# Kernel optimization log

Measured on AMD Instinct MI355X. Metric: run time of the kernel, lower is better.

Reference implementation:

```python
import jax, jax.numpy as jnp
import numpy as np

B, Q, C, H, N, D, F = 1, 2048, 2048, 1024, 16, 64, 4096
R = Q + C  # relative position encoding length
EPS = 1e-12
NEG = 1e30


def setup_inputs() -> dict:
    key = jax.random.key(0)
    ks = jax.random.split(key, 16)
    s = 0.02
    return dict(
        content_stream=jax.random.normal(ks[0], (B, Q, H), jnp.float32),
        content_mask=jnp.zeros((B, 1, Q, C), jnp.float32),
        context=jax.random.normal(ks[1], (B, C, H), jnp.float32),
        position_encoding=jax.random.normal(ks[2], (B, R, H), jnp.float32),
        content_bias=jax.random.normal(ks[3], (N, D), jnp.float32) * s,
        position_bias=jax.random.normal(ks[4], (N, D), jnp.float32) * s,
        segment_encoding=jax.random.normal(ks[5], (2, N, D), jnp.float32) * s,
        segment_matrix=jax.random.randint(ks[6], (B, Q, C), 0, 2).astype(bool),
        segment_bias=jax.random.normal(ks[7], (N, D), jnp.float32) * s,
        Wq=jax.random.normal(ks[8], (H, N, D), jnp.float32) * s,
        Wk=jax.random.normal(ks[9], (H, N, D), jnp.float32) * s,
        Wv=jax.random.normal(ks[10], (H, N, D), jnp.float32) * s,
        Wr=jax.random.normal(ks[11], (H, N, D), jnp.float32) * s,
        Wo=jax.random.normal(ks[12], (H, N, D), jnp.float32) * s,
        ln1_gamma=jnp.ones((H,), jnp.float32),
        ln1_beta=jnp.zeros((H,), jnp.float32),
        W1=jax.random.normal(ks[13], (H, F), jnp.float32) * s,
        b1=jnp.zeros((F,), jnp.float32),
        W2=jax.random.normal(ks[14], (F, H), jnp.float32) * s,
        b2=jnp.zeros((H,), jnp.float32),
        ln2_gamma=jnp.ones((H,), jnp.float32),
        ln2_beta=jnp.zeros((H,), jnp.float32),
    )


def _layernorm(x, g, b):
    m = jnp.mean(x, axis=-1, keepdims=True)
    v = jnp.mean(jnp.square(x - m), axis=-1, keepdims=True)
    return (x - m) * jax.lax.rsqrt(v + EPS) * g + b


def _rel_shift(x, klen):
    # x: [b, n, q, r] -> shifted [b, n, q, klen] (XLNet reshape trick)
    b, n, q, r = x.shape
    x = x.reshape(b, n, r, q)[:, :, 1:, :].reshape(b, n, q, r - 1)
    return x[:, :, :, :klen]


def reference(content_stream, content_mask, context, position_encoding,
              content_bias, position_bias, segment_encoding, segment_matrix,
              segment_bias, Wq, Wk, Wv, Wr, Wo, ln1_gamma, ln1_beta,
              W1, b1, W2, b2, ln2_gamma, ln2_beta):
    q = jnp.einsum('bqh,hnd->bqnd', content_stream, Wq)
    k = jnp.einsum('bch,hnd->bcnd', context, Wk)
    v = jnp.einsum('bch,hnd->bcnd', context, Wv)
    r = jnp.einsum('brh,hnd->brnd', position_encoding, Wr)

    # content / position / segment bias terms (XLNet relative attention)
    ac = jnp.einsum('bqnd,bcnd->bnqc', q + content_bias, k)
    bd = _rel_shift(jnp.einsum('bqnd,brnd->bnqr', q + position_bias, r),
                    k.shape[1])
    ef = jnp.einsum('bqnd,snd->bnqs', q + segment_bias, segment_encoding)
    ef = jnp.where(segment_matrix[:, None], ef[..., 1:], ef[..., :1])

    scores = (ac + bd + ef) / jnp.sqrt(jnp.float32(D))
    scores = scores - NEG * content_mask  # mask: 1.0 = disallowed
    probs = jax.nn.softmax(scores, axis=-1)

    attn = jnp.einsum('bnqc,bcnd->bqnd', probs, v)
    attn_out = jnp.einsum('bqnd,hnd->bqh', attn, Wo)

    # residual + LN, then FFN, residual + LN (dropout off: training=False)
    ffn_in = _layernorm(attn_out + content_stream, ln1_gamma, ln1_beta)
    ffn_out = jax.nn.relu(ffn_in @ W1 + b1) @ W2 + b2
    return _layernorm(ffn_out + ffn_in, ln2_gamma, ln2_beta)
```

## Files before the change

### kernel.cpp

```cpp
#include <hip/hip_runtime.h>
#include <stdint.h>


typedef unsigned short ushort_t;
typedef __attribute__((ext_vector_type(8))) short bf16x8;
typedef __attribute__((ext_vector_type(4))) float f32x4;

#define QLEN 2048
#define CLEN 2048
#define HDIM 1024
#define NHEAD 16
#define DHEAD 64
#define RLEN 4096
#define FDIM 4096

__device__ __forceinline__ float bf2f(ushort_t u) {
  union { float f; uint32_t i; } x; x.i = ((uint32_t)u) << 16; return x.f;
}
__device__ __forceinline__ ushort_t f2bf(float f) {
  union { float f; uint32_t i; } x; x.f = f;
  uint32_t r = x.i + 0x7fffu + ((x.i >> 16) & 1u);
  return (ushort_t)(r >> 16);
}
__device__ __forceinline__ f32x4 mfma16(bf16x8 a, bf16x8 b, f32x4 c) {
  return __builtin_amdgcn_mfma_f32_16x16x32_bf16(a, b, c, 0, 0, 0);
}
__device__ __forceinline__ bool probe_bf16(const uint32_t* probe) {
  return probe[0] == 0x3F803F80u;
}

typedef const __attribute__((address_space(1))) void* gas_t;
typedef __attribute__((address_space(3))) void* las_t;
__device__ __forceinline__ void glds16(const void* g, void* l) {
  __builtin_amdgcn_global_load_lds((gas_t)(uintptr_t)g, (las_t)(uintptr_t)l, 16, 0, 0);
}

__device__ __forceinline__ void bar_lds() {
  __asm__ volatile("s_waitcnt lgkmcnt(0)\n\ts_barrier" ::: "memory");
}
__device__ __forceinline__ void bar_full() {
  __asm__ volatile("s_waitcnt vmcnt(0) lgkmcnt(0)\n\ts_barrier" ::: "memory");
}

struct ConvJobs {
  const void* src[5];
  const void* mask_src;
  ushort_t* dst[5];
  int n[5];
  int blk0[6];
};

__global__ __launch_bounds__(256) void conv_all(
    ConvJobs J, const uint32_t* __restrict__ probe)
{
  const bool isb = probe_bf16(probe);
  int j = 0;
  #pragma unroll
  for (int t = 1; t < 5; t++) if ((int)blockIdx.x >= J.blk0[t]) j = t;
  const int lb = blockIdx.x - J.blk0[j];
  const int nb = J.blk0[j + 1] - J.blk0[j];
  const int n = J.n[j];
  ushort_t* dst = J.dst[j];
  if (j < 4) {
    const void* src = J.src[j];
    for (int i = lb * 256 + threadIdx.x; i < n; i += nb * 256)
      dst[i] = isb ? ((const ushort_t*)src)[i] : f2bf(((const float*)src)[i]);
  } else {
    const void* sm = J.src[4];
    uint32_t sw = 0;
    #pragma unroll
    for (int t = 0; t < 8; t++) sw |= ((const uint32_t*)sm)[t];
    const bool i8 = sw > 1u;
    for (int i = lb * 256 + threadIdx.x; i < n; i += nb * 256) {
      const int s = i8 ? (int)((const unsigned char*)sm)[i]
                       : (int)((const uint32_t*)sm)[i];
      const float mv = isb ? bf2f(((const ushort_t*)J.mask_src)[i])
                           : ((const float*)J.mask_src)[i];
      const float f = (float)(s ? 1 : 0) + (mv != 0.f ? 2.f : 0.f);
      dst[i] = f2bf(f);
    }
  }
}

struct SmallBatch {
  const void* src[10];
  int n[10];
  int off[10];
};

__global__ __launch_bounds__(256) void convert_small(
    SmallBatch sb, ushort_t* __restrict__ dst, const uint32_t* __restrict__ probe)
{
  const bool isb = probe_bf16(probe);
  const int t = blockIdx.x;
  const void* s = sb.src[t];
  ushort_t* d = dst + sb.off[t];
  for (int i = threadIdx.x; i < sb.n[t]; i += 256)
    d[i] = isb ? ((const ushort_t*)s)[i] : f2bf(((const float*)s)[i]);
}

struct TransJobs { const void* src[4]; ushort_t* dst[4]; };
__global__ __launch_bounds__(256) void transpose4_to_bf16(
    TransJobs T, int R, int C, const uint32_t* __restrict__ probe)
{
  const bool isb = probe_bf16(probe);
  const void* in = T.src[blockIdx.z];
  ushort_t* out = T.dst[blockIdx.z];
  __shared__ ushort_t t[32][33];
  const int bx = blockIdx.x * 32, by = blockIdx.y * 32;
  const int x = threadIdx.x & 31, y0 = threadIdx.x >> 5;
  #pragma unroll
  for (int yy = 0; yy < 32; yy += 8) {
    const size_t idx = (size_t)(by + y0 + yy) * C + bx + x;
    t[y0 + yy][x] = isb ? ((const ushort_t*)in)[idx] : f2bf(((const float*)in)[idx]);
  }
  __syncthreads();
  #pragma unroll
  for (int yy = 0; yy < 32; yy += 8)
    out[(size_t)(bx + y0 + yy) * R + by + x] = t[x][y0 + yy];
}

__global__ __launch_bounds__(256) void transpose_to_bf16(
    const void* __restrict__ in, ushort_t* __restrict__ out, int R, int C,
    const uint32_t* __restrict__ probe)
{
  const bool isb = probe_bf16(probe);
  __shared__ ushort_t t[32][33];
  const int bx = blockIdx.x * 32, by = blockIdx.y * 32;
  const int x = threadIdx.x & 31, y0 = threadIdx.x >> 5;
  #pragma unroll
  for (int yy = 0; yy < 32; yy += 8) {
    const size_t idx = (size_t)(by + y0 + yy) * C + bx + x;
    t[y0 + yy][x] = isb ? ((const ushort_t*)in)[idx] : f2bf(((const float*)in)[idx]);
  }
  __syncthreads();
  #pragma unroll
  for (int yy = 0; yy < 32; yy += 8)
    out[(size_t)(bx + y0 + yy) * R + by + x] = t[x][y0 + yy];
}

__device__ __forceinline__ void gemm_store(
    void* out, const ushort_t* bias, int M, int N, int epi,
    int gm, int gn, float v)
{
  if (epi == 0) {
    ((ushort_t*)out)[(size_t)gm * N + gn] = f2bf(v);
  } else if (epi == 1) {
    ((ushort_t*)out)[(size_t)gn * M + gm] = f2bf(v);
  } else if (epi == 2) {
    ((float*)out)[(size_t)gm * N + gn] = v;
  } else if (epi == 3) {
    v += bf2f(bias[gn]); v = v > 0.f ? v : 0.f;
    ((ushort_t*)out)[(size_t)gm * N + gn] = f2bf(v);
  } else if (epi == 4) {
    v += bf2f(bias[gn]);
    ((float*)out)[(size_t)gm * N + gn] = v;
  } else {
    ((ushort_t*)out)[((size_t)(gn >> 6) * M + gm) * 64 + (gn & 63)] = f2bf(v);
  }
}

__global__ __launch_bounds__(256) void gemm_bt_kernel(
    const ushort_t* __restrict__ A, const ushort_t* __restrict__ Bt,
    const ushort_t* __restrict__ bias, void* __restrict__ out,
    int M, int N, int K, int epi)
{
  __shared__ __attribute__((aligned(16))) ushort_t As[128 * 32];
  __shared__ __attribute__((aligned(16))) ushort_t Bs[64 * 32];
  const int tid = threadIdx.x;
  const int lane = tid & 63, wave = tid >> 6;
  const int l15 = lane & 15, quad = lane >> 4;
  const int m0 = blockIdx.y * 128, n0 = blockIdx.x * 64;

  const int arow = tid >> 2;
  const int acol = (tid & 3) * 8;

  f32x4 acc[2][4];
  #pragma unroll
  for (int i = 0; i < 2; i++)
    #pragma unroll
    for (int j = 0; j < 4; j++) acc[i][j] = (f32x4){0.f, 0.f, 0.f, 0.f};

  for (int k0 = 0; k0 < K; k0 += 32) {
    glds16(&A[(size_t)(m0 + arow) * K + k0 + acol], &As[tid * 8]);
    glds16(&A[(size_t)(m0 + arow + 64) * K + k0 + acol], &As[tid * 8 + 2048]);
    glds16(&Bt[(size_t)(n0 + arow) * K + k0 + acol], &Bs[tid * 8]);
    __syncthreads();
    bf16x8 af[2], bfr[4];
    #pragma unroll
    for (int i = 0; i < 2; i++)
      af[i] = *(const bf16x8*)&As[(wave * 32 + i * 16 + l15) * 32 + quad * 8];
    #pragma unroll
    for (int j = 0; j < 4; j++)
      bfr[j] = *(const bf16x8*)&Bs[(j * 16 + l15) * 32 + quad * 8];
    #pragma unroll
    for (int i = 0; i < 2; i++)
      #pragma unroll
      for (int j = 0; j < 4; j++)
        acc[i][j] = mfma16(af[i], bfr[j], acc[i][j]);
    __syncthreads();
  }

  #pragma unroll
  for (int i = 0; i < 2; i++)
    #pragma unroll
    for (int j = 0; j < 4; j++)
      #pragma unroll
      for (int rg = 0; rg < 4; rg++)
        gemm_store(out, bias, M, N, epi,
                   m0 + wave * 32 + i * 16 + quad * 4 + rg,
                   n0 + j * 16 + l15, acc[i][j][rg]);
}

__global__ __launch_bounds__(256) void gemm64_bt_kernel(
    const ushort_t* __restrict__ A, const ushort_t* __restrict__ Bt,
    const ushort_t* __restrict__ bias, void* __restrict__ out,
    int M, int N, int K, int epi)
{
  __shared__ __attribute__((aligned(16))) ushort_t As[64 * 32];
  __shared__ __attribute__((aligned(16))) ushort_t Bs[64 * 32];
  const int tid = threadIdx.x;
  const int lane = tid & 63, wave = tid >> 6;
  const int l15 = lane & 15, quad = lane >> 4;
  const int wm = wave >> 1, wn = wave & 1;
  const int m0 = blockIdx.y * 64, n0 = blockIdx.x * 64;

  const int arow = tid >> 2;
  const int acol = (tid & 3) * 8;

  f32x4 acc[2][2];
  #pragma unroll
  for (int i = 0; i < 2; i++)
    #pragma unroll
    for (int j = 0; j < 2; j++) acc[i][j] = (f32x4){0.f, 0.f, 0.f, 0.f};

  for (int k0 = 0; k0 < K; k0 += 32) {
    glds16(&A[(size_t)(m0 + arow) * K + k0 + acol], &As[tid * 8]);
    glds16(&Bt[(size_t)(n0 + arow) * K + k0 + acol], &Bs[tid * 8]);
    __syncthreads();
    bf16x8 af[2], bfr[2];
    #pragma unroll
    for (int i = 0; i < 2; i++)
      af[i] = *(const bf16x8*)&As[(wm * 32 + i * 16 + l15) * 32 + quad * 8];
    #pragma unroll
    for (int j = 0; j < 2; j++)
      bfr[j] = *(const bf16x8*)&Bs[(wn * 32 + j * 16 + l15) * 32 + quad * 8];
    #pragma unroll
    for (int i = 0; i < 2; i++)
      #pragma unroll
      for (int j = 0; j < 2; j++)
        acc[i][j] = mfma16(af[i], bfr[j], acc[i][j]);
    __syncthreads();
  }

  #pragma unroll
  for (int i = 0; i < 2; i++)
    #pragma unroll
    for (int j = 0; j < 2; j++)
      #pragma unroll
      for (int rg = 0; rg < 4; rg++)
        gemm_store(out, bias, M, N, epi,
                   m0 + wm * 32 + i * 16 + quad * 4 + rg,
                   n0 + wn * 32 + j * 16 + l15, acc[i][j][rg]);
}

#define ESTR 36
#define PSTR2 72
__global__ __launch_bounds__(256, 2) void attn_flash(
    const ushort_t* __restrict__ qh, const ushort_t* __restrict__ kh,
    const ushort_t* __restrict__ vT, const ushort_t* __restrict__ rh,
    const ushort_t* __restrict__ cbias, const ushort_t* __restrict__ pbias,
    const ushort_t* __restrict__ sbias, const ushort_t* __restrict__ senc,
    const ushort_t* __restrict__ fmb, ushort_t* __restrict__ attn)
{
  __shared__ __attribute__((aligned(16))) ushort_t kbuf[2][64 * 64];
  __shared__ __attribute__((aligned(16))) ushort_t vbuf[2][64 * 64];
  __shared__ __attribute__((aligned(16))) ushort_t rbuf[2][80 * 64];
  __shared__ __attribute__((aligned(16))) ushort_t Pbuf[16 * PSTR2];
  __shared__ __attribute__((aligned(16))) float escr[4][16 * ESTR];
  __shared__ __attribute__((aligned(16))) ushort_t qpc[16 * 64];
  __shared__ __attribute__((aligned(16))) ushort_t qpp[16 * 64];
  __shared__ float wsum[4][16];
  __shared__ float e0s[16], e1s[16];

  const int n = blockIdx.x;
  const int q0 = blockIdx.y * 16;
  const int tid = threadIdx.x;
  const int lane = tid & 63, wave = tid >> 6;
  const int l15 = lane & 15, quad = lane >> 4;

  const ushort_t* qn = qh + (size_t)n * QLEN * 64;
  const ushort_t* kn = kh + (size_t)n * CLEN * 64;
  const ushort_t* rn = rh + (size_t)n * RLEN * 64;
  const ushort_t* vn = vT + (size_t)n * 64 * CLEN;

  const int srow = lane >> 3;
  const int sg = (lane & 7) ^ srow;

  for (int idx = tid; idx < 16 * 64; idx += 256) {
    const int row = idx >> 6, col = idx & 63;
    const float qv = bf2f(qn[(size_t)(q0 + row) * 64 + col]);
    qpc[idx] = f2bf(qv + bf2f(cbias[n * DHEAD + col]));
    qpp[idx] = f2bf(qv + bf2f(pbias[n * DHEAD + col]));
  }
  if (tid < 32) {
    const int row = tid & 15, sidx = tid >> 4;
    float a = 0.f;
    for (int d = 0; d < DHEAD; d++)
      a += (bf2f(qn[(size_t)(q0 + row) * 64 + d]) + bf2f(sbias[n * DHEAD + d]))
           * bf2f(senc[(size_t)(sidx * NHEAD + n) * DHEAD + d]);
    if (sidx == 0) e0s[row] = a; else e1s[row] = a;
  }

  {
    const int c0 = 0, ua = c0 - q0 + (QLEN - 16);
    if (wave == 0) {
      #pragma unroll
      for (int i = 0; i < 8; i++)
        glds16(kn + (size_t)(c0 + i * 8 + srow) * 64 + sg * 8, &kbuf[0][i * 512]);
    } else if (wave == 1) {
      #pragma unroll
      for (int i = 0; i < 8; i++)
        glds16(vn + (size_t)(i * 8 + srow) * CLEN + c0 + sg * 8, &vbuf[0][i * 512]);
    } else if (wave == 2) {
      #pragma unroll
      for (int i = 0; i < 8; i++)
        glds16(rn + (size_t)(ua + i * 8 + srow) * 64 + sg * 8, &rbuf[0][i * 512]);
    } else {
      #pragma unroll
      for (int i = 0; i < 2; i++)
        glds16(rn + (size_t)(ua + 64 + i * 8 + srow) * 64 + sg * 8, &rbuf[0][(64 + i * 8) * 64]);
    }
  }
  bar_full();

  const bf16x8* qpc8 = (const bf16x8*)qpc;
  const bf16x8* qpp8 = (const bf16x8*)qpp;
  const bf16x8 qc0 = qpc8[l15 * 8 + quad];
  const bf16x8 qc1 = qpc8[l15 * 8 + 4 + quad];
  const bf16x8 qp0 = qpp8[l15 * 8 + quad];
  const bf16x8 qp1 = qpp8[l15 * 8 + 4 + quad];
  const float a0_ = e0s[l15] * 0.125f;
  const float ad_ = (e1s[l15] - e0s[l15]) * 0.125f;

  float* escr_w = escr[wave];
  const int gk0 = quad ^ (l15 & 7);
  const int gk1 = (quad + 4) ^ (l15 & 7);

  float l_row = 0.f;
  f32x4 O = (f32x4){0.f, 0.f, 0.f, 0.f};

  for (int ci = 0; ci < CLEN / 64; ci++) {
    const int b = ci & 1;
    const int c0 = ci * 64;

    if (ci + 1 < CLEN / 64) {
      const int c1 = c0 + 64, ua1 = c1 - q0 + (QLEN - 16);
      if (wave == 0) {
        #pragma unroll
        for (int i = 0; i < 8; i++)
          glds16(kn + (size_t)(c1 + i * 8 + srow) * 64 + sg * 8, &kbuf[b ^ 1][i * 512]);
      } else if (wave == 1) {
        #pragma unroll
        for (int i = 0; i < 8; i++)
          glds16(vn + (size_t)(i * 8 + srow) * CLEN + c1 + sg * 8, &vbuf[b ^ 1][i * 512]);
      } else if (wave == 2) {
        #pragma unroll
        for (int i = 0; i < 8; i++)
          glds16(rn + (size_t)(ua1 + i * 8 + srow) * 64 + sg * 8, &rbuf[b ^ 1][i * 512]);
      } else {
        #pragma unroll
        for (int i = 0; i < 2; i++)
          glds16(rn + (size_t)(ua1 + 64 + i * 8 + srow) * 64 + sg * 8, &rbuf[b ^ 1][(64 + i * 8) * 64]);
      }
    }

    const size_t eoff = (size_t)(q0 + l15) * CLEN + c0 + wave * 16 + quad * 4;
    const uint2 fmv = *(const uint2*)&fmb[eoff];

    #pragma unroll
    for (int t = 0; t < 2; t++) {
      const int rrow = (wave + t) * 16 + l15;
      f32x4 e = (f32x4){0.f, 0.f, 0.f, 0.f};
      e = mfma16(*(const bf16x8*)&rbuf[b][rrow * 64 + gk0 * 8], qp0, e);
      e = mfma16(*(const bf16x8*)&rbuf[b][rrow * 64 + gk1 * 8], qp1, e);
      *(f32x4*)&escr_w[l15 * ESTR + t * 16 + quad * 4] = e;
    }

    const int krow = wave * 16 + l15;
    f32x4 a = (f32x4){0.f, 0.f, 0.f, 0.f};
    a = mfma16(*(const bf16x8*)&kbuf[b][krow * 64 + gk0 * 8], qc0, a);
    a = mfma16(*(const bf16x8*)&kbuf[b][krow * 64 + gk1 * 8], qc1, a);

    const ushort_t fm4[4] = {(ushort_t)(fmv.x & 0xffff), (ushort_t)(fmv.x >> 16),
                             (ushort_t)(fmv.y & 0xffff), (ushort_t)(fmv.y >> 16)};
    const float* dg = &escr_w[l15 * ESTR + quad * 4 - l15 + 16];
    float p[4], psum = 0.f;
    #pragma unroll
    for (int rg = 0; rg < 4; rg++) {
      const float f = bf2f(fm4[rg]);
      const float mk = floorf(f * 0.5f);
      const float sm = f - 2.f * mk;
      float v = fmaf(a[rg] + dg[rg], 0.125f, fmaf(sm, ad_, a0_));
      v = fmaf(mk, -1.0e30f, v);
      p[rg] = __expf(v);
      psum += p[rg];
    }
    psum += __shfl_xor(psum, 16);
    psum += __shfl_xor(psum, 32);
    l_row += psum;

    {
      uint2 pk;
      pk.x = (uint32_t)f2bf(p[0]) | ((uint32_t)f2bf(p[1]) << 16);
      pk.y = (uint32_t)f2bf(p[2]) | ((uint32_t)f2bf(p[3]) << 16);
      *(uint2*)&Pbuf[l15 * PSTR2 + wave * 16 + quad * 4] = pk;
    }
    bar_lds();

    const bf16x8 pa0 = *(const bf16x8*)&Pbuf[l15 * PSTR2 + quad * 8];
    const bf16x8 pa1 = *(const bf16x8*)&Pbuf[l15 * PSTR2 + 32 + quad * 8];
    const int vrow = wave * 16 + l15;
    O = mfma16(pa0, *(const bf16x8*)&vbuf[b][vrow * 64 + gk0 * 8], O);
    O = mfma16(pa1, *(const bf16x8*)&vbuf[b][vrow * 64 + gk1 * 8], O);

    bar_full();
  }

  if (quad == 0) wsum[wave][l15] = l_row;
  __syncthreads();
  const float l = wsum[0][l15] + wsum[1][l15] + wsum[2][l15] + wsum[3][l15];
  const float linv = 1.0f / l;
  float linv4[4];
  #pragma unroll
  for (int rg = 0; rg < 4; rg++) linv4[rg] = __shfl(linv, quad * 4 + rg);
  #pragma unroll
  for (int rg = 0; rg < 4; rg++)
    attn[(size_t)(q0 + quad * 4 + rg) * HDIM + n * 64 + wave * 16 + l15] =
        f2bf(O[rg] * linv4[rg]);
}

__global__ __launch_bounds__(256) void ln_kernel(
    const float* __restrict__ x, const ushort_t* __restrict__ res_bf,
    const float* __restrict__ res_f, const ushort_t* __restrict__ gamma,
    const ushort_t* __restrict__ beta, ushort_t* __restrict__ out_bf,
    float* __restrict__ out_f, void* __restrict__ out_dyn,
    const uint32_t* __restrict__ probe)
{
  const int row = blockIdx.x, tid = threadIdx.x;
  const int lane = tid & 63, wave = tid >> 6;
  __shared__ float red[8];
  const size_t base = (size_t)row * HDIM;
  float v[4];
  #pragma unroll
  for (int i = 0; i < 4; i++) {
    const int h = tid + i * 256;
    const float rv = res_bf ? bf2f(res_bf[base + h]) : res_f[base + h];
    v[i] = x[base + h] + rv;
  }
  float s = v[0] + v[1] + v[2] + v[3];
  float ss = v[0] * v[0] + v[1] * v[1] + v[2] * v[2] + v[3] * v[3];
  #pragma unroll
  for (int off = 32; off > 0; off >>= 1) {
    s += __shfl_xor(s, off);
    ss += __shfl_xor(ss, off);
  }
  if (lane == 0) { red[wave] = s; red[4 + wave] = ss; }
  __syncthreads();
  s = red[0] + red[1] + red[2] + red[3];
  ss = red[4] + red[5] + red[6] + red[7];
  const float mean = s * (1.0f / HDIM);
  float var = ss * (1.0f / HDIM) - mean * mean;
  var = var > 0.f ? var : 0.f;
  const float rs = rsqrtf(var + 1e-12f);
  const bool outb = out_dyn ? probe_bf16(probe) : false;
  #pragma unroll
  for (int i = 0; i < 4; i++) {
    const int h = tid + i * 256;
    const float y = (v[i] - mean) * rs * bf2f(gamma[h]) + bf2f(beta[h]);
    if (out_bf) out_bf[base + h] = f2bf(y);
    if (out_f)  out_f[base + h] = y;
    if (out_dyn) {
      if (outb) ((ushort_t*)out_dyn)[base + h] = f2bf(y);
      else      ((float*)out_dyn)[base + h] = y;
    }
  }
}

extern "C" void kernel_launch(void* const* d_in, const int* in_sizes, int n_in,
                              void* d_out, int out_size, void* d_ws, size_t ws_size,
                              hipStream_t stream)
{
  (void)in_sizes; (void)n_in; (void)out_size; (void)ws_size;

  const void* cs_r   = d_in[0];
  const void* mask_r = d_in[1];
  const void* ctx_r  = d_in[2];
  const void* pe_r   = d_in[3];
  const void* cb_r   = d_in[4];
  const void* pb_r   = d_in[5];
  const void* senc_r = d_in[6];
  const void* smat   = d_in[7];
  const void* sb_r   = d_in[8];
  const void* Wq_r   = d_in[9];
  const void* Wk_r   = d_in[10];
  const void* Wv_r   = d_in[11];
  const void* Wr_r   = d_in[12];
  const void* Wo_r   = d_in[13];
  const void* g1_r   = d_in[14];
  const void* be1_r  = d_in[15];
  const void* W1_r   = d_in[16];
  const void* b1_r   = d_in[17];
  const void* W2_r   = d_in[18];
  const void* b2_r   = d_in[19];
  const void* g2_r   = d_in[20];
  const void* be2_r  = d_in[21];

  const uint32_t* probe = (const uint32_t*)g1_r;

  char* w = (char*)d_ws;
  #define WSOFF(mb) ((void*)(w + ((size_t)(mb) << 20)))
  ushort_t* fm_b     = (ushort_t*)WSOFF(0);
  ushort_t* Wqt      = (ushort_t*)WSOFF(8);
  ushort_t* Wkt      = (ushort_t*)WSOFF(10);
  ushort_t* Wvt      = (ushort_t*)WSOFF(12);
  ushort_t* Wrt      = (ushort_t*)WSOFF(14);
  ushort_t* W1t      = (ushort_t*)WSOFF(16);
  ushort_t* W2t      = (ushort_t*)WSOFF(24);
  ushort_t* Wo_b     = (ushort_t*)WSOFF(32);
  ushort_t* smalls   = (ushort_t*)WSOFF(34);
  ushort_t* cs_b     = (ushort_t*)WSOFF(35);
  ushort_t* ctx_b    = (ushort_t*)WSOFF(47);
  ushort_t* pe_b     = (ushort_t*)WSOFF(51);
  ushort_t* qbuf     = (ushort_t*)WSOFF(59);
  ushort_t* kbuf     = (ushort_t*)WSOFF(63);
  ushort_t* vTbuf    = (ushort_t*)WSOFF(67);
  ushort_t* rbuf     = (ushort_t*)WSOFF(71);
  ushort_t* attnbuf  = (ushort_t*)WSOFF(79);
  float*    attn_out = (float*)WSOFF(83);
  ushort_t* ffn_in_b = (ushort_t*)WSOFF(91);
  ushort_t* hidden   = (ushort_t*)WSOFF(39);
  float*    ffn_in_f = (float*)WSOFF(71);
  float*    ffn_out  = (float*)WSOFF(83);

  ushort_t* cb   = smalls + 0;
  ushort_t* pb   = smalls + 1024;
  ushort_t* sb   = smalls + 2048;
  ushort_t* senc = smalls + 3072;
  ushort_t* b1   = smalls + 5120;
  ushort_t* b2   = smalls + 9216;
  ushort_t* g1   = smalls + 10240;
  ushort_t* be1  = smalls + 11264;
  ushort_t* g2   = smalls + 12288;
  ushort_t* be2  = smalls + 13312;

  const dim3 blk(256);

  SmallBatch sbatch;
  const void* ssrc[10] = {cb_r, pb_r, sb_r, senc_r, b1_r, b2_r, g1_r, be1_r, g2_r, be2_r};
  const int   sn[10]   = {1024, 1024, 1024, 2048, 4096, 1024, 1024, 1024, 1024, 1024};
  const int   soff[10] = {0, 1024, 2048, 3072, 5120, 9216, 10240, 11264, 12288, 13312};
  for (int i = 0; i < 10; i++) { sbatch.src[i] = ssrc[i]; sbatch.n[i] = sn[i]; sbatch.off[i] = soff[i]; }
  convert_small<<<10, blk, 0, stream>>>(sbatch, smalls, probe);

  ConvJobs cj;
  cj.src[0] = cs_r;  cj.dst[0] = cs_b;  cj.n[0] = QLEN * HDIM;
  cj.src[1] = ctx_r; cj.dst[1] = ctx_b; cj.n[1] = CLEN * HDIM;
  cj.src[2] = pe_r;  cj.dst[2] = pe_b;  cj.n[2] = RLEN * HDIM;
  cj.src[3] = Wo_r;  cj.dst[3] = Wo_b;  cj.n[3] = HDIM * HDIM;
  cj.src[4] = smat;  cj.dst[4] = fm_b;  cj.n[4] = QLEN * CLEN;
  cj.mask_src = mask_r;
  int pfx = 0;
  for (int i = 0; i < 5; i++) {
    cj.blk0[i] = pfx;
    pfx += (cj.n[i] + 2047) / 2048;
  }
  cj.blk0[5] = pfx;
  conv_all<<<pfx, blk, 0, stream>>>(cj, probe);

  TransJobs tj;
  tj.src[0] = Wq_r; tj.dst[0] = Wqt;
  tj.src[1] = Wk_r; tj.dst[1] = Wkt;
  tj.src[2] = Wv_r; tj.dst[2] = Wvt;
  tj.src[3] = Wr_r; tj.dst[3] = Wrt;
  transpose4_to_bf16<<<dim3(32, 32, 4), blk, 0, stream>>>(tj, HDIM, HDIM, probe);
  transpose_to_bf16<<<dim3(128, 32), blk, 0, stream>>>(W1_r, W1t, HDIM, FDIM, probe);
  transpose_to_bf16<<<dim3(32, 128), blk, 0, stream>>>(W2_r, W2t, FDIM, HDIM, probe);

  gemm64_bt_kernel<<<dim3(16, 32), blk, 0, stream>>>(cs_b,  Wqt, nullptr, qbuf,  QLEN, HDIM, HDIM, 5);
  gemm64_bt_kernel<<<dim3(16, 32), blk, 0, stream>>>(ctx_b, Wkt, nullptr, kbuf,  CLEN, HDIM, HDIM, 5);
  gemm64_bt_kernel<<<dim3(16, 32), blk, 0, stream>>>(ctx_b, Wvt, nullptr, vTbuf, CLEN, HDIM, HDIM, 1);
  gemm_bt_kernel<<<dim3(16, 32), blk, 0, stream>>>(pe_b,  Wrt, nullptr, rbuf,  RLEN, HDIM, HDIM, 5);

  attn_flash<<<dim3(NHEAD, QLEN / 16), blk, 0, stream>>>(
      qbuf, kbuf, vTbuf, rbuf, cb, pb, sb, senc, fm_b, attnbuf);

  gemm64_bt_kernel<<<dim3(16, 32), blk, 0, stream>>>(attnbuf, Wo_b, nullptr, attn_out, QLEN, HDIM, HDIM, 2);

  ln_kernel<<<QLEN, blk, 0, stream>>>(attn_out, cs_b, nullptr, g1, be1,
                                      ffn_in_b, ffn_in_f, nullptr, probe);

  gemm_bt_kernel<<<dim3(64, 16), blk, 0, stream>>>(ffn_in_b, W1t, b1, hidden,  QLEN, FDIM, HDIM, 3);
  gemm64_bt_kernel<<<dim3(16, 32), blk, 0, stream>>>(hidden, W2t, b2, ffn_out, QLEN, HDIM, FDIM, 4);

  ln_kernel<<<QLEN, blk, 0, stream>>>(ffn_out, nullptr, ffn_in_f, g2, be2,
                                      nullptr, nullptr, d_out, probe);
  #undef WSOFF
}
```

Baseline: 547.7 us.

## Fuse K/V projections, use 128x128 tile for FFN1, prefetch attention mask

```diff
diff --git a/kernel.cpp b/kernel.cpp
--- a/kernel.cpp
+++ b/kernel.cpp
@@ -155,8 +155,13 @@
   } else if (epi == 4) {
     v += bf2f(bias[gn]);
     ((float*)out)[(size_t)gm * N + gn] = v;
+  } else if (epi == 5) {
+    ((ushort_t*)out)[((size_t)(gn >> 6) * M + gm) * 64 + (gn & 63)] = f2bf(v);
   } else {
-    ((ushort_t*)out)[((size_t)(gn >> 6) * M + gm) * 64 + (gn & 63)] = f2bf(v);
+    if (gn < 1024)
+      ((ushort_t*)out)[((size_t)(gn >> 6) * M + gm) * 64 + (gn & 63)] = f2bf(v);
+    else
+      ((ushort_t*)out)[(size_t)2097152 + (size_t)(gn - 1024) * M + gm] = f2bf(v);
   }
 }
 
@@ -210,6 +215,60 @@
         gemm_store(out, bias, M, N, epi,
                    m0 + wave * 32 + i * 16 + quad * 4 + rg,
                    n0 + j * 16 + l15, acc[i][j][rg]);
+}
+
+__global__ __launch_bounds__(256) void gemm128_bt_kernel(
+    const ushort_t* __restrict__ A, const ushort_t* __restrict__ Bt,
+    const ushort_t* __restrict__ bias, void* __restrict__ out,
+    int M, int N, int K, int epi)
+{
+  __shared__ __attribute__((aligned(16))) ushort_t As[128 * 32];
+  __shared__ __attribute__((aligned(16))) ushort_t Bs[128 * 32];
+  const int tid = threadIdx.x;
+  const int lane = tid & 63, wave = tid >> 6;
+  const int l15 = lane & 15, quad = lane >> 4;
+  const int wm = wave >> 1, wn = wave & 1;
+  const int m0 = blockIdx.y * 128, n0 = blockIdx.x * 128;
+
+  const int arow = tid >> 2;
+  const int acol = (tid & 3) * 8;
+
+  f32x4 acc[4][4];
+  #pragma unroll
+  for (int i = 0; i < 4; i++)
+    #pragma unroll
+    for (int j = 0; j < 4; j++) acc[i][j] = (f32x4){0.f, 0.f, 0.f, 0.f};
+
+  for (int k0 = 0; k0 < K; k0 += 32) {
+    glds16(&A[(size_t)(m0 + arow) * K + k0 + acol], &As[tid * 8]);
+    glds16(&A[(size_t)(m0 + arow + 64) * K + k0 + acol], &As[tid * 8 + 2048]);
+    glds16(&Bt[(size_t)(n0 + arow) * K + k0 + acol], &Bs[tid * 8]);
+    glds16(&Bt[(size_t)(n0 + arow + 64) * K + k0 + acol], &Bs[tid * 8 + 2048]);
+    __syncthreads();
+    bf16x8 af[4], bfr[4];
+    #pragma unroll
+    for (int i = 0; i < 4; i++)
+      af[i] = *(const bf16x8*)&As[(wm * 64 + i * 16 + l15) * 32 + quad * 8];
+    #pragma unroll
+    for (int j = 0; j < 4; j++)
+      bfr[j] = *(const bf16x8*)&Bs[(wn * 64 + j * 16 + l15) * 32 + quad * 8];
+    #pragma unroll
+    for (int i = 0; i < 4; i++)
+      #pragma unroll
+      for (int j = 0; j < 4; j++)
+        acc[i][j] = mfma16(af[i], bfr[j], acc[i][j]);
+    __syncthreads();
+  }
+
+  #pragma unroll
+  for (int i = 0; i < 4; i++)
+    #pragma unroll
+    for (int j = 0; j < 4; j++)
+      #pragma unroll
+      for (int rg = 0; rg < 4; rg++)
+        gemm_store(out, bias, M, N, epi,
+                   m0 + wm * 64 + i * 16 + quad * 4 + rg,
+                   n0 + wn * 64 + j * 16 + l15, acc[i][j][rg]);
 }
 
 __global__ __launch_bounds__(256) void gemm64_bt_kernel(
@@ -297,6 +356,9 @@
   const int srow = lane >> 3;
   const int sg = (lane & 7) ^ srow;
 
+  const size_t eoff_base = (size_t)(q0 + l15) * CLEN + wave * 16 + quad * 4;
+  uint2 fmv = *(const uint2*)&fmb[eoff_base];
+
   for (int idx = tid; idx < 16 * 64; idx += 256) {
     const int row = idx >> 6, col = idx & 63;
     const float qv = bf2f(qn[(size_t)(q0 + row) * 64 + col]);
@@ -352,10 +414,10 @@
 
   for (int ci = 0; ci < CLEN / 64; ci++) {
     const int b = ci & 1;
-    const int c0 = ci * 64;
-
+
+    uint2 fmv_next = fmv;
     if (ci + 1 < CLEN / 64) {
-      const int c1 = c0 + 64, ua1 = c1 - q0 + (QLEN - 16);
+      const int c1 = (ci + 1) * 64, ua1 = c1 - q0 + (QLEN - 16);
       if (wave == 0) {
         #pragma unroll
         for (int i = 0; i < 8; i++)
@@ -373,10 +435,8 @@
         for (int i = 0; i < 2; i++)
           glds16(rn + (size_t)(ua1 + 64 + i * 8 + srow) * 64 + sg * 8, &rbuf[b ^ 1][(64 + i * 8) * 64]);
       }
+      fmv_next = *(const uint2*)&fmb[eoff_base + (size_t)(ci + 1) * 64];
     }
-
-    const size_t eoff = (size_t)(q0 + l15) * CLEN + c0 + wave * 16 + quad * 4;
-    const uint2 fmv = *(const uint2*)&fmb[eoff];
 
     #pragma unroll
     for (int t = 0; t < 2; t++) {
@@ -425,6 +485,7 @@
     O = mfma16(pa1, *(const bf16x8*)&vbuf[b][vrow * 64 + gk1 * 8], O);
 
     bar_full();
+    fmv = fmv_next;
   }
 
   if (quad == 0) wsum[wave][l15] = l_row;
@@ -588,8 +649,7 @@
   transpose_to_bf16<<<dim3(32, 128), blk, 0, stream>>>(W2_r, W2t, FDIM, HDIM, probe);
 
   gemm64_bt_kernel<<<dim3(16, 32), blk, 0, stream>>>(cs_b,  Wqt, nullptr, qbuf,  QLEN, HDIM, HDIM, 5);
-  gemm64_bt_kernel<<<dim3(16, 32), blk, 0, stream>>>(ctx_b, Wkt, nullptr, kbuf,  CLEN, HDIM, HDIM, 5);
-  gemm64_bt_kernel<<<dim3(16, 32), blk, 0, stream>>>(ctx_b, Wvt, nullptr, vTbuf, CLEN, HDIM, HDIM, 1);
+  gemm_bt_kernel<<<dim3(32, 16), blk, 0, stream>>>(ctx_b, Wkt, nullptr, kbuf, CLEN, 2048, HDIM, 6);
   gemm_bt_kernel<<<dim3(16, 32), blk, 0, stream>>>(pe_b,  Wrt, nullptr, rbuf,  RLEN, HDIM, HDIM, 5);
 
   attn_flash<<<dim3(NHEAD, QLEN / 16), blk, 0, stream>>>(
@@ -600,7 +660,7 @@
   ln_kernel<<<QLEN, blk, 0, stream>>>(attn_out, cs_b, nullptr, g1, be1,
                                       ffn_in_b, ffn_in_f, nullptr, probe);
 
-  gemm_bt_kernel<<<dim3(64, 16), blk, 0, stream>>>(ffn_in_b, W1t, b1, hidden,  QLEN, FDIM, HDIM, 3);
+  gemm128_bt_kernel<<<dim3(32, 16), blk, 0, stream>>>(ffn_in_b, W1t, b1, hidden, QLEN, FDIM, HDIM, 3);
   gemm64_bt_kernel<<<dim3(16, 32), blk, 0, stream>>>(hidden, W2t, b2, ffn_out, QLEN, HDIM, FDIM, 4);
 
   ln_kernel<<<QLEN, blk, 0, stream>>>(ffn_out, nullptr, ffn_in_f, g2, be2,
```

Result: no change. 551.3 us (+0.7%).
